# Kernel tuning notes

Hardware: AMD Instinct MI355X
Metric: run time of the kernel (lower is better)

Reference implementation:

```python
import jax, jax.numpy as jnp
import numpy as np

N = 100000      # n_nodes
E = 1600000     # n_edges (avg degree 16)
F_IN = 128      # nfeat
H = 128         # nhid
C = 64          # nclass


def setup_inputs() -> dict:
    key = jax.random.key(0)
    ks = jax.random.split(key, 6)
    x = jax.random.normal(ks[0], (N, F_IN), dtype=jnp.float32)
    edge_index = jax.random.randint(ks[1], (2, E), 0, N, dtype=jnp.int32)
    # Glorot-ish init for GCNConv weights, zeros for bias (PyG default)
    W1 = jax.random.normal(ks[2], (F_IN, H), dtype=jnp.float32) * (1.0 / np.sqrt(F_IN))
    b1 = jnp.zeros((H,), dtype=jnp.float32)
    W2 = jax.random.normal(ks[3], (H, C), dtype=jnp.float32) * (1.0 / np.sqrt(H))
    b2 = jnp.zeros((C,), dtype=jnp.float32)
    return {"x": x, "edge_index": edge_index, "W1": W1, "b1": b1, "W2": W2, "b2": b2}


def _gcn_conv(x, W, b, src, dst, n):
    """PyG GCNConv: h = W^T x, out_i = sum_j norm_ij * h_j + b, with
    symmetric normalization over the self-loop-augmented graph."""
    h = x @ W                                                   # [n, out]
    deg = jax.ops.segment_sum(jnp.ones(src.shape[0], h.dtype), dst, num_segments=n)
    dinv = jnp.where(deg > 0, jax.lax.rsqrt(deg), 0.0)          # D^-1/2
    norm = dinv[src] * dinv[dst]                                # [E+n]
    msg = h[src] * norm[:, None]                                # gather + scale
    out = jax.ops.segment_sum(msg, dst, num_segments=n)         # scatter-add
    return out + b


def reference(x, edge_index, W1, b1, W2, b2):
    loop = jnp.arange(N, dtype=edge_index.dtype)
    src = jnp.concatenate([edge_index[0], loop])  # sources j (with self loops)
    dst = jnp.concatenate([edge_index[1], loop])  # targets i
    h = jax.nn.relu(_gcn_conv(x, W1, b1, src, dst, N))  # dropout = identity (eval)
    out = _gcn_conv(h, W2, b2, src, dst, N)
    return jax.nn.log_softmax(out, axis=1)
```

## Files before the change

### kernel.cpp

```cpp
#include <hip/hip_runtime.h>
#include <hip/hip_fp16.h>
#include <cstdint>
#include <cstddef>
#include <cstring>


__device__ inline unsigned pack_bf16x2(float a, float b) {
    unsigned ua = __float_as_uint(a);
    unsigned ub = __float_as_uint(b);
    ua += 0x7fffu + ((ua >> 16) & 1u);
    ub += 0x7fffu + ((ub >> 16) & 1u);
    return (ua >> 16) | (ub & 0xffff0000u);
}
__device__ inline unsigned short bf16_rne(float v) {
    unsigned u = __float_as_uint(v);
    u += 0x7fffu + ((u >> 16) & 1u);
    return (unsigned short)(u >> 16);
}
__device__ inline float bf16lo(unsigned u) { return __uint_as_float(u << 16); }
__device__ inline float bf16hi(unsigned u) { return __uint_as_float(u & 0xffff0000u); }


typedef float fv2 __attribute__((ext_vector_type(2)));

template <bool HI>
__device__ inline fv2 fp8_fv2(unsigned u) {
#if __has_builtin(__builtin_amdgcn_cvt_pk_f32_fp8)
    return __builtin_amdgcn_cvt_pk_f32_fp8((int)u, HI);
#else
    unsigned u2 = HI ? (u >> 16) : (u & 0xffffu);
    unsigned w = (u2 & 0xFFu) | ((u2 & 0xFF00u) << 8);
    unsigned hb = ((w & 0x00800080u) << 8) | ((w & 0x007f007fu) << 7);
    __half2 h2;
    memcpy(&h2, &hb, 4);
    float2 f = __half22float2(h2);
    fv2 r;
    r.x = f.x * 256.0f;
    r.y = f.y * 256.0f;
    return r;
#endif
}

__device__ inline fv2 bfpair(unsigned u) {
    union { unsigned q[2]; fv2 f; } t;
    t.q[0] = u << 16;
    t.q[1] = u & 0xffff0000u;
    return t.f;
}

__device__ inline unsigned f32_to_fp8_byte(float v) {
    unsigned short hb = __half_as_ushort(__float2half(v * 0.00390625f));
    unsigned t = hb & 0x7fffu;
    t += 0x3fu + ((t >> 7) & 1u);
    return ((hb >> 8) & 0x80u) | (t >> 7);
}

__device__ inline unsigned char f32_to_fp8_b(float v) {
#if __has_builtin(__builtin_amdgcn_cvt_pk_fp8_f32)
    return (unsigned char)(__builtin_amdgcn_cvt_pk_fp8_f32(v, v, 0, false) & 0xff);
#else
    return (unsigned char)f32_to_fp8_byte(v);
#endif
}

typedef int iv4 __attribute__((ext_vector_type(4)));

#define NPART 8
#define KB    32
#define NPP_MAX 12500


__global__ void k_zero16(int* __restrict__ p) {
    if (threadIdx.x < 16) p[threadIdx.x] = 0;
}

__global__ __launch_bounds__(256) void k_bcount(const int* __restrict__ dst,
                                                int* __restrict__ bucketCount,
                                                int E, int npp) {
    __shared__ int c8[NPART];
    if (threadIdx.x < NPART) c8[threadIdx.x] = 0;
    __syncthreads();
    int t = blockIdx.x * blockDim.x + threadIdx.x;
    int stride = gridDim.x * blockDim.x;
    int E4 = E >> 2;
    const iv4* d4 = (const iv4*)dst;
    for (int i = t; i < E4; i += stride) {
        iv4 d = d4[i];
        atomicAdd(&c8[(unsigned)d.x / (unsigned)npp], 1);
        atomicAdd(&c8[(unsigned)d.y / (unsigned)npp], 1);
        atomicAdd(&c8[(unsigned)d.z / (unsigned)npp], 1);
        atomicAdd(&c8[(unsigned)d.w / (unsigned)npp], 1);
    }
    for (int e = E4 * 4 + t; e < E; e += stride)
        atomicAdd(&c8[(unsigned)dst[e] / (unsigned)npp], 1);
    __syncthreads();
    if (threadIdx.x < NPART) atomicAdd(&bucketCount[threadIdx.x], c8[threadIdx.x]);
}

__global__ void k_bscan(const int* __restrict__ bucketCount,
                        int* __restrict__ bucketBase,
                        int* __restrict__ bucketCursor) {
    if (threadIdx.x == 0) {
        int run = 0;
        for (int p = 0; p < NPART; ++p) {
            bucketBase[p] = run;
            bucketCursor[p] = run;
            run += bucketCount[p];
        }
    }
}

__global__ __launch_bounds__(256) void k_bucket(const int* __restrict__ src,
                                                const int* __restrict__ dst,
                                                int* __restrict__ bucketCursor,
                                                int2* __restrict__ pairs,
                                                int E, int npp) {
    __shared__ int cnt8[NPART], run8[NPART], gbase8[NPART];
    int tid = threadIdx.x;
    int base_e = blockIdx.x * 4096 + tid * 16;
    int nv = min(16, E - base_e);
    if (nv < 0) nv = 0;
    int dv[16], sv[16];
    if (nv == 16) {
        for (int q = 0; q < 4; ++q) {
            iv4 d = *(const iv4*)(dst + base_e + q * 4);
            iv4 s = *(const iv4*)(src + base_e + q * 4);
            dv[q * 4 + 0] = d.x; dv[q * 4 + 1] = d.y; dv[q * 4 + 2] = d.z; dv[q * 4 + 3] = d.w;
            sv[q * 4 + 0] = s.x; sv[q * 4 + 1] = s.y; sv[q * 4 + 2] = s.z; sv[q * 4 + 3] = s.w;
        }
    } else {
        for (int k = 0; k < nv; ++k) { dv[k] = dst[base_e + k]; sv[k] = src[base_e + k]; }
    }
    if (tid < NPART) { cnt8[tid] = 0; run8[tid] = 0; }
    __syncthreads();
    for (int k = 0; k < nv; ++k)
        atomicAdd(&cnt8[(unsigned)dv[k] / (unsigned)npp], 1);
    __syncthreads();
    if (tid < NPART) gbase8[tid] = atomicAdd(&bucketCursor[tid], cnt8[tid]);
    __syncthreads();
    for (int k = 0; k < nv; ++k) {
        int p = (unsigned)dv[k] / (unsigned)npp;
        int r = atomicAdd(&run8[p], 1);
        int2 pr; pr.x = dv[k]; pr.y = sv[k];
        pairs[gbase8[p] + r] = pr;
    }
}

__global__ __launch_bounds__(256) void k_count_part(const int2* __restrict__ pairs,
                                                    const int* __restrict__ bucketBase,
                                                    const int* __restrict__ bucketCount,
                                                    int* __restrict__ cntarr, int npp) {
    __shared__ int h[NPP_MAX];
    int p = blockIdx.x & (NPART - 1);
    int b = blockIdx.x >> 3;
    int lo = p * npp;
    for (int i = threadIdx.x; i < npp; i += 256) h[i] = 0;
    __syncthreads();
    int segBase = bucketBase[p], sz = bucketCount[p];
    int chunk = (sz + KB - 1) / KB;
    int s0 = segBase + b * chunk;
    int s1 = min(segBase + sz, s0 + chunk);
    for (int i = s0 + threadIdx.x; i < s1; i += 256)
        atomicAdd(&h[pairs[i].x - lo], 1);
    __syncthreads();
    size_t out = (size_t)(p * KB + b) * npp;
    for (int i = threadIdx.x; i < npp; i += 256) cntarr[out + i] = h[i];
}

__global__ void k_indeg_scan(const int* __restrict__ cntarr,
                             float* __restrict__ dinv,
                             int* __restrict__ row_ptr,
                             int* __restrict__ partials, int n, int npp) {
    __shared__ int s[256];
    int t = threadIdx.x;
    int node0 = blockIdx.x * 1024 + t * 4;
    int v0 = 0, v1 = 0, v2 = 0, v3 = 0;
    if (((npp & 3) == 0) && (node0 + 3 < n) && (node0 / npp == (node0 + 3) / npp)) {
        int p = node0 / npp;
        int dl = node0 - p * npp;
        size_t base = (size_t)p * KB * npp + dl;
        for (int b = 0; b < KB; ++b) {
            iv4 c = *(const iv4*)(cntarr + base + (size_t)b * npp);
            v0 += c.x; v1 += c.y; v2 += c.z; v3 += c.w;
        }
    } else {
        for (int r = 0; r < 4; ++r) {
            int node = node0 + r;
            if (node < n) {
                int p = node / npp;
                int dl = node - p * npp;
                size_t base = (size_t)p * KB * npp + dl;
                int sum = 0;
                for (int b = 0; b < KB; ++b) sum += cntarr[base + (size_t)b * npp];
                if (r == 0) v0 = sum; else if (r == 1) v1 = sum;
                else if (r == 2) v2 = sum; else v3 = sum;
            }
        }
    }
    if (node0 + 0 < n) dinv[node0 + 0] = rsqrtf((float)v0 + 1.0f);
    if (node0 + 1 < n) dinv[node0 + 1] = rsqrtf((float)v1 + 1.0f);
    if (node0 + 2 < n) dinv[node0 + 2] = rsqrtf((float)v2 + 1.0f);
    if (node0 + 3 < n) dinv[node0 + 3] = rsqrtf((float)v3 + 1.0f);
    int sum = v0 + v1 + v2 + v3;
    s[t] = sum;
    __syncthreads();
    for (int off = 1; off < 256; off <<= 1) {
        int x = (t >= off) ? s[t - off] : 0;
        __syncthreads();
        s[t] += x;
        __syncthreads();
    }
    int excl = s[t] - sum;
    if ((node0 + 0) < n) row_ptr[node0 + 0] = excl;
    if ((node0 + 1) < n) row_ptr[node0 + 1] = excl + v0;
    if ((node0 + 2) < n) row_ptr[node0 + 2] = excl + v0 + v1;
    if ((node0 + 3) < n) row_ptr[node0 + 3] = excl + v0 + v1 + v2;
    if (t == 255) partials[blockIdx.x] = s[255];
}

__global__ void k_scan_partials(int* __restrict__ partials, int np) {
    __shared__ int s[256];
    int t = threadIdx.x;
    int v = (t < np) ? partials[t] : 0;
    s[t] = v;
    __syncthreads();
    for (int off = 1; off < 256; off <<= 1) {
        int x = (t >= off) ? s[t - off] : 0;
        __syncthreads();
        s[t] += x;
        __syncthreads();
    }
    if (t < np) partials[t] = s[t] - v;
}

__global__ void k_finalize_bases(int* __restrict__ row_ptr,
                                 const int* __restrict__ partials,
                                 int* __restrict__ cntarr, int n, int E, int npp) {
    int i = blockIdx.x * blockDim.x + threadIdx.x;
    if (i >= n) return;
    int rp = row_ptr[i] + partials[i >> 10];
    row_ptr[i] = rp;
    if (i == 0) row_ptr[n] = E;
    int p = (unsigned)i / (unsigned)npp;
    int dl = i - p * npp;
    size_t base = (size_t)p * KB * npp + dl;
    int run = rp;
    for (int b = 0; b < KB; ++b) {
        size_t idx = base + (size_t)b * npp;
        int c = cntarr[idx];
        cntarr[idx] = run;
        run += c;
    }
}

__global__ __launch_bounds__(256) void k_fill2(const int2* __restrict__ pairs,
                                               const int* __restrict__ bucketBase,
                                               const int* __restrict__ bucketCount,
                                               const int* __restrict__ cntarr,
                                               int* __restrict__ col, int npp) {
    __shared__ int cur[NPP_MAX];
    int p = blockIdx.x & (NPART - 1);
    int b = blockIdx.x >> 3;
    int lo = p * npp;
    size_t slice = (size_t)(p * KB + b) * npp;
    for (int i = threadIdx.x; i < npp; i += 256) cur[i] = cntarr[slice + i];
    __syncthreads();
    int segBase = bucketBase[p], sz = bucketCount[p];
    int chunk = (sz + KB - 1) / KB;
    int s0 = segBase + b * chunk;
    int s1 = min(segBase + sz, s0 + chunk);
    for (int i = s0 + threadIdx.x; i < s1; i += 256) {
        int2 e = pairs[i];
        int pos = atomicAdd(&cur[e.x - lo], 1);
        col[pos] = e.y;
    }
}

typedef __attribute__((ext_vector_type(8))) short short8;
typedef __attribute__((ext_vector_type(4))) float f32x4;

union FragU {
    short8 s;
    uint4 u4;
    unsigned u[4];
};

template <int NOUT>
__global__ void k_packW(const float* __restrict__ W, unsigned* __restrict__ Bp) {
    const int NT = NOUT / 16;
    int nf = 4 * NT * 64;
    for (int fid = threadIdx.x; fid < nf; fid += 256) {
        int q = fid / (NT * 64);
        int rem = fid - q * NT * 64;
        int nt = rem >> 6;
        int lane = rem & 63;
        int k0 = q * 32 + (lane >> 4) * 8;
        int ncol = nt * 16 + (lane & 15);
        unsigned u[4];
        for (int h = 0; h < 4; ++h) {
            float a = W[(k0 + 2 * h) * NOUT + ncol];
            float b = W[(k0 + 2 * h + 1) * NOUT + ncol];
            u[h] = pack_bf16x2(a, b);
        }
        uint4 o = {u[0], u[1], u[2], u[3]};
        *(uint4*)(Bp + (size_t)fid * 4) = o;
    }
}

__global__ __launch_bounds__(256) void k_gemm128_mfma(const float* __restrict__ X,
                                                      const unsigned* __restrict__ Bp,
                                                      const float* __restrict__ dinv,
                                                      unsigned char* __restrict__ H8,
                                                      int n) {
    int w = threadIdx.x >> 6;
    int lane = threadIdx.x & 63;
    int quad = lane >> 4;
    int lrow = lane & 15;
    int row0 = blockIdx.x * 64 + w * 16;
    int rowA = min(row0 + lrow, n - 1);

    f32x4 acc[8];
    for (int nt = 0; nt < 8; ++nt) acc[nt] = (f32x4){0.f, 0.f, 0.f, 0.f};

    for (int q = 0; q < 4; ++q) {
        const float* xp = X + (size_t)rowA * 128 + q * 32 + quad * 8;
        float4 x0 = *(const float4*)xp;
        float4 x1 = *(const float4*)(xp + 4);
        FragU a;
        a.u[0] = pack_bf16x2(x0.x, x0.y);
        a.u[1] = pack_bf16x2(x0.z, x0.w);
        a.u[2] = pack_bf16x2(x1.x, x1.y);
        a.u[3] = pack_bf16x2(x1.z, x1.w);
        for (int nt = 0; nt < 8; ++nt) {
            FragU b;
            b.u4 = *(const uint4*)(Bp + ((size_t)(q * 8 + nt) * 64 + lane) * 4);
            acc[nt] = __builtin_amdgcn_mfma_f32_16x16x32_bf16(a.s, b.s, acc[nt], 0, 0, 0);
        }
    }

    int rbase = row0 + quad * 4;
    float dv[4];
    if (rbase + 3 < n) {
        float4 d4 = *(const float4*)(dinv + rbase);
        dv[0] = d4.x; dv[1] = d4.y; dv[2] = d4.z; dv[3] = d4.w;
    } else {
        for (int r = 0; r < 4; ++r) dv[r] = dinv[min(rbase + r, n - 1)];
    }
    for (int nt = 0; nt < 8; ++nt) {
        for (int r = 0; r < 4; ++r) {
            int row = rbase + r;
            if (row < n)
                H8[(size_t)row * 128 + nt * 16 + lrow] = f32_to_fp8_b(dv[r] * acc[nt][r]);
        }
    }
}

__global__ __launch_bounds__(256) void k_gemm64_mfma(const unsigned* __restrict__ Xb,
                                                     const unsigned* __restrict__ Bp,
                                                     const float* __restrict__ dinv,
                                                     unsigned short* __restrict__ H16,
                                                     int n) {
    int w = threadIdx.x >> 6;
    int lane = threadIdx.x & 63;
    int quad = lane >> 4;
    int lrow = lane & 15;
    int row0 = blockIdx.x * 64 + w * 16;
    int rowA = min(row0 + lrow, n - 1);

    f32x4 acc[4];
    for (int nt = 0; nt < 4; ++nt) acc[nt] = (f32x4){0.f, 0.f, 0.f, 0.f};

    for (int q = 0; q < 4; ++q) {
        FragU a;
        a.u4 = *(const uint4*)(Xb + (size_t)rowA * 64 + q * 16 + quad * 4);
        for (int nt = 0; nt < 4; ++nt) {
            FragU b;
            b.u4 = *(const uint4*)(Bp + ((size_t)(q * 4 + nt) * 64 + lane) * 4);
            acc[nt] = __builtin_amdgcn_mfma_f32_16x16x32_bf16(a.s, b.s, acc[nt], 0, 0, 0);
        }
    }

    int rbase = row0 + quad * 4;
    float dv[4];
    if (rbase + 3 < n) {
        float4 d4 = *(const float4*)(dinv + rbase);
        dv[0] = d4.x; dv[1] = d4.y; dv[2] = d4.z; dv[3] = d4.w;
    } else {
        for (int r = 0; r < 4; ++r) dv[r] = dinv[min(rbase + r, n - 1)];
    }
    for (int nt = 0; nt < 4; ++nt) {
        for (int r = 0; r < 4; ++r) {
            int row = rbase + r;
            if (row < n)
                H16[(size_t)row * 64 + nt * 16 + lrow] = bf16_rne(dv[r] * acc[nt][r]);
        }
    }
}


__global__ __launch_bounds__(256) void k_agg_relu(const unsigned* __restrict__ hs,
                                                  const float* __restrict__ dinv,
                                                  const int* __restrict__ row_ptr,
                                                  const int* __restrict__ col,
                                                  const float* __restrict__ bias,
                                                  unsigned* __restrict__ out, int n) {
    int node = blockIdx.x * 16 + (threadIdx.x >> 4);
    if (node >= n) return;
    int l = threadIdx.x & 15;
    const uint2* hrow = (const uint2*)hs;
    fv2 a0 = {0.f, 0.f}, a1 = {0.f, 0.f}, a2 = {0.f, 0.f}, a3 = {0.f, 0.f};
    {
        uint2 u = hrow[(size_t)node * 16 + l];
        a0 += fp8_fv2<false>(u.x); a1 += fp8_fv2<true>(u.x);
        a2 += fp8_fv2<false>(u.y); a3 += fp8_fv2<true>(u.y);
    }
    int k = row_ptr[node], p1 = row_ptr[node + 1];
    for (; k + 8 <= p1; k += 8) {
        int cA = col[k + 0], cB = col[k + 1], cC = col[k + 2], cD = col[k + 3];
        int cE = col[k + 4], cF = col[k + 5], cG = col[k + 6], cH = col[k + 7];
        uint2 uA = hrow[(size_t)cA * 16 + l];
        uint2 uB = hrow[(size_t)cB * 16 + l];
        uint2 uC = hrow[(size_t)cC * 16 + l];
        uint2 uD = hrow[(size_t)cD * 16 + l];
        uint2 uE = hrow[(size_t)cE * 16 + l];
        uint2 uF = hrow[(size_t)cF * 16 + l];
        uint2 uG = hrow[(size_t)cG * 16 + l];
        uint2 uH = hrow[(size_t)cH * 16 + l];
        a0 += fp8_fv2<false>(uA.x); a1 += fp8_fv2<true>(uA.x);
        a2 += fp8_fv2<false>(uA.y); a3 += fp8_fv2<true>(uA.y);
        a0 += fp8_fv2<false>(uB.x); a1 += fp8_fv2<true>(uB.x);
        a2 += fp8_fv2<false>(uB.y); a3 += fp8_fv2<true>(uB.y);
        a0 += fp8_fv2<false>(uC.x); a1 += fp8_fv2<true>(uC.x);
        a2 += fp8_fv2<false>(uC.y); a3 += fp8_fv2<true>(uC.y);
        a0 += fp8_fv2<false>(uD.x); a1 += fp8_fv2<true>(uD.x);
        a2 += fp8_fv2<false>(uD.y); a3 += fp8_fv2<true>(uD.y);
        a0 += fp8_fv2<false>(uE.x); a1 += fp8_fv2<true>(uE.x);
        a2 += fp8_fv2<false>(uE.y); a3 += fp8_fv2<true>(uE.y);
        a0 += fp8_fv2<false>(uF.x); a1 += fp8_fv2<true>(uF.x);
        a2 += fp8_fv2<false>(uF.y); a3 += fp8_fv2<true>(uF.y);
        a0 += fp8_fv2<false>(uG.x); a1 += fp8_fv2<true>(uG.x);
        a2 += fp8_fv2<false>(uG.y); a3 += fp8_fv2<true>(uG.y);
        a0 += fp8_fv2<false>(uH.x); a1 += fp8_fv2<true>(uH.x);
        a2 += fp8_fv2<false>(uH.y); a3 += fp8_fv2<true>(uH.y);
    }
    for (; k + 4 <= p1; k += 4) {
        int cA = col[k + 0], cB = col[k + 1], cC = col[k + 2], cD = col[k + 3];
        uint2 uA = hrow[(size_t)cA * 16 + l];
        uint2 uB = hrow[(size_t)cB * 16 + l];
        uint2 uC = hrow[(size_t)cC * 16 + l];
        uint2 uD = hrow[(size_t)cD * 16 + l];
        a0 += fp8_fv2<false>(uA.x); a1 += fp8_fv2<true>(uA.x);
        a2 += fp8_fv2<false>(uA.y); a3 += fp8_fv2<true>(uA.y);
        a0 += fp8_fv2<false>(uB.x); a1 += fp8_fv2<true>(uB.x);
        a2 += fp8_fv2<false>(uB.y); a3 += fp8_fv2<true>(uB.y);
        a0 += fp8_fv2<false>(uC.x); a1 += fp8_fv2<true>(uC.x);
        a2 += fp8_fv2<false>(uC.y); a3 += fp8_fv2<true>(uC.y);
        a0 += fp8_fv2<false>(uD.x); a1 += fp8_fv2<true>(uD.x);
        a2 += fp8_fv2<false>(uD.y); a3 += fp8_fv2<true>(uD.y);
    }
    for (; k < p1; ++k) {
        int j = col[k];
        uint2 u = hrow[(size_t)j * 16 + l];
        a0 += fp8_fv2<false>(u.x); a1 += fp8_fv2<true>(u.x);
        a2 += fp8_fv2<false>(u.y); a3 += fp8_fv2<true>(u.y);
    }
    float di = dinv[node];
    float4 b4a = *(const float4*)(bias + 8 * l);
    float4 b4b = *(const float4*)(bias + 8 * l + 4);
    float v0 = fmaf(di, a0.x, b4a.x);
    float v1 = fmaf(di, a0.y, b4a.y);
    float v2 = fmaf(di, a1.x, b4a.z);
    float v3 = fmaf(di, a1.y, b4a.w);
    float v4 = fmaf(di, a2.x, b4b.x);
    float v5 = fmaf(di, a2.y, b4b.y);
    float v6 = fmaf(di, a3.x, b4b.z);
    float v7 = fmaf(di, a3.y, b4b.w);
    v0 = v0 > 0.f ? v0 : 0.f;
    v1 = v1 > 0.f ? v1 : 0.f;
    v2 = v2 > 0.f ? v2 : 0.f;
    v3 = v3 > 0.f ? v3 : 0.f;
    v4 = v4 > 0.f ? v4 : 0.f;
    v5 = v5 > 0.f ? v5 : 0.f;
    v6 = v6 > 0.f ? v6 : 0.f;
    v7 = v7 > 0.f ? v7 : 0.f;
    uint4 o = {pack_bf16x2(v0, v1), pack_bf16x2(v2, v3),
               pack_bf16x2(v4, v5), pack_bf16x2(v6, v7)};
    *(uint4*)(out + (size_t)node * 64 + 4 * l) = o;
}

__global__ __launch_bounds__(256) void k_agg_lsm(const unsigned* __restrict__ hs,
                                                 const float* __restrict__ dinv,
                                                 const int* __restrict__ row_ptr,
                                                 const int* __restrict__ col,
                                                 const float* __restrict__ bias,
                                                 float* __restrict__ out, int n) {
    int node = blockIdx.x * 16 + (threadIdx.x >> 4);
    if (node >= n) return;
    int l = threadIdx.x & 15;
    const uint2* hrow = (const uint2*)hs;
    fv2 aX = {0.f, 0.f}, aY = {0.f, 0.f};
    {
        uint2 u = hrow[(size_t)node * 16 + l];
        aX += bfpair(u.x);
        aY += bfpair(u.y);
    }
    int k = row_ptr[node], p1 = row_ptr[node + 1];
    for (; k + 8 <= p1; k += 8) {
        int cA = col[k + 0], cB = col[k + 1], cC = col[k + 2], cD = col[k + 3];
        int cE = col[k + 4], cF = col[k + 5], cG = col[k + 6], cH = col[k + 7];
        uint2 uA = hrow[(size_t)cA * 16 + l];
        uint2 uB = hrow[(size_t)cB * 16 + l];
        uint2 uC = hrow[(size_t)cC * 16 + l];
        uint2 uD = hrow[(size_t)cD * 16 + l];
        uint2 uE = hrow[(size_t)cE * 16 + l];
        uint2 uF = hrow[(size_t)cF * 16 + l];
        uint2 uG = hrow[(size_t)cG * 16 + l];
        uint2 uH = hrow[(size_t)cH * 16 + l];
        aX += bfpair(uA.x); aY += bfpair(uA.y);
        aX += bfpair(uB.x); aY += bfpair(uB.y);
        aX += bfpair(uC.x); aY += bfpair(uC.y);
        aX += bfpair(uD.x); aY += bfpair(uD.y);
        aX += bfpair(uE.x); aY += bfpair(uE.y);
        aX += bfpair(uF.x); aY += bfpair(uF.y);
        aX += bfpair(uG.x); aY += bfpair(uG.y);
        aX += bfpair(uH.x); aY += bfpair(uH.y);
    }
    for (; k + 4 <= p1; k += 4) {
        int cA = col[k + 0], cB = col[k + 1], cC = col[k + 2], cD = col[k + 3];
        uint2 uA = hrow[(size_t)cA * 16 + l];
        uint2 uB = hrow[(size_t)cB * 16 + l];
        uint2 uC = hrow[(size_t)cC * 16 + l];
        uint2 uD = hrow[(size_t)cD * 16 + l];
        aX += bfpair(uA.x); aY += bfpair(uA.y);
        aX += bfpair(uB.x); aY += bfpair(uB.y);
        aX += bfpair(uC.x); aY += bfpair(uC.y);
        aX += bfpair(uD.x); aY += bfpair(uD.y);
    }
    for (; k < p1; ++k) {
        int j = col[k];
        uint2 u = hrow[(size_t)j * 16 + l];
        aX += bfpair(u.x); aY += bfpair(u.y);
    }
    float di = dinv[node];
    float4 b4 = *(const float4*)(bias + 4 * l);
    float v0 = fmaf(di, aX.x, b4.x);
    float v1 = fmaf(di, aX.y, b4.y);
    float v2 = fmaf(di, aY.x, b4.z);
    float v3 = fmaf(di, aY.y, b4.w);
    float m = fmaxf(fmaxf(v0, v1), fmaxf(v2, v3));
    for (int off = 8; off; off >>= 1) m = fmaxf(m, __shfl_xor(m, off));
    float s = __expf(v0 - m) + __expf(v1 - m) + __expf(v2 - m) + __expf(v3 - m);
    for (int off = 8; off; off >>= 1) s += __shfl_xor(s, off);
    float ls = __logf(s);
    float4 o = {v0 - m - ls, v1 - m - ls, v2 - m - ls, v3 - m - ls};
    *(float4*)(out + (size_t)node * 64 + 4 * l) = o;
}


extern "C" void kernel_launch(void* const* d_in, const int* in_sizes, int n_in,
                              void* d_out, int out_size, void* d_ws, size_t ws_size,
                              hipStream_t stream) {
    const float* x  = (const float*)d_in[0];
    const int*   ei = (const int*)d_in[1];
    const float* W1 = (const float*)d_in[2];
    const float* b1 = (const float*)d_in[3];
    const float* W2 = (const float*)d_in[4];
    const float* b2 = (const float*)d_in[5];
    float* out = (float*)d_out;

    const int N = in_sizes[0] / 128;
    const int E = in_sizes[1] / 2;
    const int* src = ei;
    const int* dst = ei + E;
    const int npp = (N + NPART - 1) / NPART;

    char* w = (char*)d_ws;
    size_t off = 0;
    auto alloc = [&](size_t bytes) -> void* {
        void* p = w + off;
        off += (bytes + 255) & ~(size_t)255;
        return p;
    };
    int*      row_ptr  = (int*)alloc((size_t)(N + 1) * 4);
    int*      colarr   = (int*)alloc((size_t)E * 4);
    int*      partials = (int*)alloc(256 * 4);
    int*      bmeta    = (int*)alloc(16 * 4);
    int*      bbase    = (int*)alloc(NPART * 4);
    float*    dinv     = (float*)alloc((size_t)N * 4);
    unsigned* h1f8     = (unsigned*)alloc((size_t)N * 32 * 4);
    unsigned* a1b      = (unsigned*)alloc((size_t)N * 64 * 4);
    unsigned* h2b      = (unsigned*)alloc((size_t)N * 32 * 4);
    unsigned* Bp1      = (unsigned*)alloc(4 * 8 * 64 * 16);
    unsigned* Bp2      = (unsigned*)alloc(4 * 4 * 64 * 16);
    int2* pairs  = (int2*)a1b;
    int*  cntarr = (int*)((char*)a1b + (size_t)E * 8);
    (void)ws_size; (void)n_in; (void)out_size;

    int* bucketCount  = bmeta;
    int* bucketCursor = bmeta + 8;
    int nscan = (N + 1023) / 1024;
    int nA3 = (E + 4095) / 4096;
    int ngemm = (N + 63) / 64;

    k_zero16<<<1, 64, 0, stream>>>(bmeta);
    k_packW<128><<<1, 256, 0, stream>>>(W1, Bp1);
    k_packW<64><<<1, 256, 0, stream>>>(W2, Bp2);
    k_bcount<<<256, 256, 0, stream>>>(dst, bucketCount, E, npp);
    k_bscan<<<1, 64, 0, stream>>>(bucketCount, bbase, bucketCursor);
    k_bucket<<<nA3, 256, 0, stream>>>(src, dst, bucketCursor, pairs, E, npp);
    k_count_part<<<NPART * KB, 256, 0, stream>>>(pairs, bbase, bucketCount, cntarr, npp);
    k_indeg_scan<<<nscan, 256, 0, stream>>>(cntarr, dinv, row_ptr, partials, N, npp);
    k_scan_partials<<<1, 256, 0, stream>>>(partials, nscan);
    k_finalize_bases<<<(N + 255) / 256, 256, 0, stream>>>(row_ptr, partials, cntarr,
                                                          N, E, npp);
    k_fill2<<<NPART * KB, 256, 0, stream>>>(pairs, bbase, bucketCount, cntarr,
                                            colarr, npp);

    k_gemm128_mfma<<<ngemm, 256, 0, stream>>>(x, Bp1, dinv, (unsigned char*)h1f8, N);
    k_agg_relu<<<(N + 15) / 16, 256, 0, stream>>>(h1f8, dinv, row_ptr, colarr, b1, a1b, N);
    k_gemm64_mfma<<<ngemm, 256, 0, stream>>>(a1b, Bp2, dinv, (unsigned short*)h2b, N);
    k_agg_lsm<<<(N + 15) / 16, 256, 0, stream>>>(h2b, dinv, row_ptr, colarr, b2, out, N);
}
```

Baseline: 274.2 us.

## Replace count-scan-bucket pipeline with single-pass ballot bucketing into fixed-capacity packed partitions

Result: no change. 269.3 us (-1.8%).

```diff
diff --git a/kernel.cpp b/kernel.cpp
--- a/kernel.cpp
+++ b/kernel.cpp
@@ -17,8 +17,6 @@
     u += 0x7fffu + ((u >> 16) & 1u);
     return (unsigned short)(u >> 16);
 }
-__device__ inline float bf16lo(unsigned u) { return __uint_as_float(u << 16); }
-__device__ inline float bf16hi(unsigned u) { return __uint_as_float(u & 0xffff0000u); }
 
 
 typedef float fv2 __attribute__((ext_vector_type(2)));
@@ -68,100 +66,99 @@
 #define NPART 8
 #define KB    32
 #define NPP_MAX 12500
-
-
-__global__ void k_zero16(int* __restrict__ p) {
-    if (threadIdx.x < 16) p[threadIdx.x] = 0;
-}
-
-__global__ __launch_bounds__(256) void k_bcount(const int* __restrict__ dst,
-                                                int* __restrict__ bucketCount,
-                                                int E, int npp) {
-    __shared__ int c8[NPART];
-    if (threadIdx.x < NPART) c8[threadIdx.x] = 0;
+#define EB    2048
+
+
+__global__ __launch_bounds__(256) void k_bucket_ballot(const int* __restrict__ src,
+                                                       const int* __restrict__ dst,
+                                                       int* __restrict__ cursor8,
+                                                       unsigned* __restrict__ pairs,
+                                                       int E, int npp, int capE,
+                                                       int srcb) {
+    __shared__ int sWcnt[4][NPART];
+    __shared__ int sWoff[4][NPART];
+    int tid = threadIdx.x;
+    int wv = tid >> 6;
+    int lane = tid & 63;
+    int base_e = blockIdx.x * EB + tid * 8;
+    int nv = min(8, E - base_e);
+    if (nv < 0) nv = 0;
+    int dv[8], sv[8];
+    if (nv == 8) {
+        *(iv4*)(dv + 0) = *(const iv4*)(dst + base_e + 0);
+        *(iv4*)(dv + 4) = *(const iv4*)(dst + base_e + 4);
+        *(iv4*)(sv + 0) = *(const iv4*)(src + base_e + 0);
+        *(iv4*)(sv + 4) = *(const iv4*)(src + base_e + 4);
+    } else {
+        for (int k = 0; k < 8; ++k) {
+            dv[k] = (k < nv) ? dst[base_e + k] : -1;
+            sv[k] = (k < nv) ? src[base_e + k] : 0;
+        }
+    }
+    unsigned long long below = (1ull << lane) - 1ull;
+    int wb[NPART];
+#pragma unroll
+    for (int pp = 0; pp < NPART; ++pp) wb[pp] = 0;
+    int pv[8], pos[8];
+#pragma unroll
+    for (int s = 0; s < 8; ++s) {
+        int d = dv[s];
+        int p = (d >= 0) ? (int)((unsigned)d / (unsigned)npp) : NPART;
+        pv[s] = p;
+        unsigned long long msel = 0;
+        int base = 0;
+#pragma unroll
+        for (int pp = 0; pp < NPART; ++pp) {
+            unsigned long long m = __ballot(p == pp);
+            if (p == pp) { msel = m; base = wb[pp]; }
+            wb[pp] += (int)__popcll(m);
+        }
+        pos[s] = base + (int)__popcll(msel & below);
+    }
+    if (lane < NPART) {
+        int v = 0;
+#pragma unroll
+        for (int pp = 0; pp < NPART; ++pp)
+            if (lane == pp) v = wb[pp];
+        sWcnt[wv][lane] = v;
+    }
     __syncthreads();
-    int t = blockIdx.x * blockDim.x + threadIdx.x;
-    int stride = gridDim.x * blockDim.x;
-    int E4 = E >> 2;
-    const iv4* d4 = (const iv4*)dst;
-    for (int i = t; i < E4; i += stride) {
-        iv4 d = d4[i];
-        atomicAdd(&c8[(unsigned)d.x / (unsigned)npp], 1);
-        atomicAdd(&c8[(unsigned)d.y / (unsigned)npp], 1);
-        atomicAdd(&c8[(unsigned)d.z / (unsigned)npp], 1);
-        atomicAdd(&c8[(unsigned)d.w / (unsigned)npp], 1);
-    }
-    for (int e = E4 * 4 + t; e < E; e += stride)
-        atomicAdd(&c8[(unsigned)dst[e] / (unsigned)npp], 1);
+    if (tid < NPART) {
+        int c0 = sWcnt[0][tid], c1 = sWcnt[1][tid], c2 = sWcnt[2][tid], c3 = sWcnt[3][tid];
+        int gb = atomicAdd(&cursor8[tid], c0 + c1 + c2 + c3);
+        sWoff[0][tid] = gb;
+        sWoff[1][tid] = gb + c0;
+        sWoff[2][tid] = gb + c0 + c1;
+        sWoff[3][tid] = gb + c0 + c1 + c2;
+    }
     __syncthreads();
-    if (threadIdx.x < NPART) atomicAdd(&bucketCount[threadIdx.x], c8[threadIdx.x]);
-}
-
-__global__ void k_bscan(const int* __restrict__ bucketCount,
-                        int* __restrict__ bucketBase,
-                        int* __restrict__ bucketCursor) {
-    if (threadIdx.x == 0) {
-        int run = 0;
-        for (int p = 0; p < NPART; ++p) {
-            bucketBase[p] = run;
-            bucketCursor[p] = run;
-            run += bucketCount[p];
-        }
-    }
-}
-
-__global__ __launch_bounds__(256) void k_bucket(const int* __restrict__ src,
-                                                const int* __restrict__ dst,
-                                                int* __restrict__ bucketCursor,
-                                                int2* __restrict__ pairs,
-                                                int E, int npp) {
-    __shared__ int cnt8[NPART], run8[NPART], gbase8[NPART];
-    int tid = threadIdx.x;
-    int base_e = blockIdx.x * 4096 + tid * 16;
-    int nv = min(16, E - base_e);
-    if (nv < 0) nv = 0;
-    int dv[16], sv[16];
-    if (nv == 16) {
-        for (int q = 0; q < 4; ++q) {
-            iv4 d = *(const iv4*)(dst + base_e + q * 4);
-            iv4 s = *(const iv4*)(src + base_e + q * 4);
-            dv[q * 4 + 0] = d.x; dv[q * 4 + 1] = d.y; dv[q * 4 + 2] = d.z; dv[q * 4 + 3] = d.w;
-            sv[q * 4 + 0] = s.x; sv[q * 4 + 1] = s.y; sv[q * 4 + 2] = s.z; sv[q * 4 + 3] = s.w;
-        }
-    } else {
-        for (int k = 0; k < nv; ++k) { dv[k] = dst[base_e + k]; sv[k] = src[base_e + k]; }
-    }
-    if (tid < NPART) { cnt8[tid] = 0; run8[tid] = 0; }
-    __syncthreads();
-    for (int k = 0; k < nv; ++k)
-        atomicAdd(&cnt8[(unsigned)dv[k] / (unsigned)npp], 1);
-    __syncthreads();
-    if (tid < NPART) gbase8[tid] = atomicAdd(&bucketCursor[tid], cnt8[tid]);
-    __syncthreads();
-    for (int k = 0; k < nv; ++k) {
-        int p = (unsigned)dv[k] / (unsigned)npp;
-        int r = atomicAdd(&run8[p], 1);
-        int2 pr; pr.x = dv[k]; pr.y = sv[k];
-        pairs[gbase8[p] + r] = pr;
-    }
-}
-
-__global__ __launch_bounds__(256) void k_count_part(const int2* __restrict__ pairs,
-                                                    const int* __restrict__ bucketBase,
-                                                    const int* __restrict__ bucketCount,
-                                                    int* __restrict__ cntarr, int npp) {
+#pragma unroll
+    for (int s = 0; s < 8; ++s) {
+        int p = pv[s];
+        if (p < NPART) {
+            int off = sWoff[wv][p];
+            pairs[(size_t)p * capE + off + pos[s]] =
+                ((unsigned)(dv[s] - p * npp) << srcb) | (unsigned)sv[s];
+        }
+    }
+}
+
+__global__ __launch_bounds__(256) void k_count_part(const unsigned* __restrict__ pairs,
+                                                    const int* __restrict__ cursor8,
+                                                    int* __restrict__ cntarr,
+                                                    int npp, int capE, int srcb) {
     __shared__ int h[NPP_MAX];
     int p = blockIdx.x & (NPART - 1);
     int b = blockIdx.x >> 3;
-    int lo = p * npp;
     for (int i = threadIdx.x; i < npp; i += 256) h[i] = 0;
     __syncthreads();
-    int segBase = bucketBase[p], sz = bucketCount[p];
+    int sz = cursor8[p];
     int chunk = (sz + KB - 1) / KB;
-    int s0 = segBase + b * chunk;
-    int s1 = min(segBase + sz, s0 + chunk);
+    int s0 = b * chunk;
+    int s1 = min(sz, s0 + chunk);
+    const unsigned* seg = pairs + (size_t)p * capE;
     for (int i = s0 + threadIdx.x; i < s1; i += 256)
-        atomicAdd(&h[pairs[i].x - lo], 1);
+        atomicAdd(&h[seg[i] >> srcb], 1);
     __syncthreads();
     size_t out = (size_t)(p * KB + b) * npp;
     for (int i = threadIdx.x; i < npp; i += 256) cntarr[out + i] = h[i];
@@ -253,26 +250,27 @@
     }
 }
 
-__global__ __launch_bounds__(256) void k_fill2(const int2* __restrict__ pairs,
-                                               const int* __restrict__ bucketBase,
-                                               const int* __restrict__ bucketCount,
+__global__ __launch_bounds__(256) void k_fill2(const unsigned* __restrict__ pairs,
+                                               const int* __restrict__ cursor8,
                                                const int* __restrict__ cntarr,
-                                               int* __restrict__ col, int npp) {
+                                               int* __restrict__ col,
+                                               int npp, int capE, int srcb) {
     __shared__ int cur[NPP_MAX];
     int p = blockIdx.x & (NPART - 1);
     int b = blockIdx.x >> 3;
-    int lo = p * npp;
     size_t slice = (size_t)(p * KB + b) * npp;
     for (int i = threadIdx.x; i < npp; i += 256) cur[i] = cntarr[slice + i];
     __syncthreads();
-    int segBase = bucketBase[p], sz = bucketCount[p];
+    int sz = cursor8[p];
     int chunk = (sz + KB - 1) / KB;
-    int s0 = segBase + b * chunk;
-    int s1 = min(segBase + sz, s0 + chunk);
+    int s0 = b * chunk;
+    int s1 = min(sz, s0 + chunk);
+    const unsigned* seg = pairs + (size_t)p * capE;
+    unsigned smask = (1u << srcb) - 1u;
     for (int i = s0 + threadIdx.x; i < s1; i += 256) {
-        int2 e = pairs[i];
-        int pos = atomicAdd(&cur[e.x - lo], 1);
-        col[pos] = e.y;
+        unsigned u = seg[i];
+        int pos = atomicAdd(&cur[u >> srcb], 1);
+        col[pos] = (int)(u & smask);
     }
 }
 
@@ -285,9 +283,8 @@
     unsigned u[4];
 };
 
-template <int NOUT>
-__global__ void k_packW(const float* __restrict__ W, unsigned* __restrict__ Bp) {
-    const int NT = NOUT / 16;
+__device__ inline void packW_body(const float* __restrict__ W, unsigned* __restrict__ Bp,
+                                  int NOUT, int NT) {
     int nf = 4 * NT * 64;
     for (int fid = threadIdx.x; fid < nf; fid += 256) {
         int q = fid / (NT * 64);
@@ -305,6 +302,12 @@
         uint4 o = {u[0], u[1], u[2], u[3]};
         *(uint4*)(Bp + (size_t)fid * 4) = o;
     }
+}
+
+__global__ void k_packW2(const float* __restrict__ W1, unsigned* __restrict__ Bp1,
+                         const float* __restrict__ W2, unsigned* __restrict__ Bp2) {
+    if (blockIdx.x == 0) packW_body(W1, Bp1, 128, 8);
+    else                 packW_body(W2, Bp2, 64, 4);
 }
 
 __global__ __launch_bounds__(256) void k_gemm128_mfma(const float* __restrict__ X,
@@ -573,6 +576,9 @@
     const int* src = ei;
     const int* dst = ei + E;
     const int npp = (N + NPART - 1) / NPART;
+    const int capE = (E + NPART - 1) / NPART + 32768;
+    int srcb = 1;
+    while ((1 << srcb) < N) ++srcb;
 
     char* w = (char*)d_ws;
     size_t off = 0;
@@ -584,37 +590,33 @@
     int*      row_ptr  = (int*)alloc((size_t)(N + 1) * 4);
     int*      colarr   = (int*)alloc((size_t)E * 4);
     int*      partials = (int*)alloc(256 * 4);
-    int*      bmeta    = (int*)alloc(16 * 4);
-    int*      bbase    = (int*)alloc(NPART * 4);
+    int*      cursor8  = (int*)alloc(8 * 4);
     float*    dinv     = (float*)alloc((size_t)N * 4);
     unsigned* h1f8     = (unsigned*)alloc((size_t)N * 32 * 4);
     unsigned* a1b      = (unsigned*)alloc((size_t)N * 64 * 4);
     unsigned* h2b      = (unsigned*)alloc((size_t)N * 32 * 4);
     unsigned* Bp1      = (unsigned*)alloc(4 * 8 * 64 * 16);
     unsigned* Bp2      = (unsigned*)alloc(4 * 4 * 64 * 16);
-    int2* pairs  = (int2*)a1b;
-    int*  cntarr = (int*)((char*)a1b + (size_t)E * 8);
+    unsigned* pairsU   = (unsigned*)a1b;
+    int*      cntarr   = (int*)((char*)a1b + (size_t)NPART * capE * 4);
     (void)ws_size; (void)n_in; (void)out_size;
 
-    int* bucketCount  = bmeta;
-    int* bucketCursor = bmeta + 8;
     int nscan = (N + 1023) / 1024;
-    int nA3 = (E + 4095) / 4096;
+    int nbb = (E + EB - 1) / EB;
     int ngemm = (N + 63) / 64;
 
-    k_zero16<<<1, 64, 0, stream>>>(bmeta);
-    k_packW<128><<<1, 256, 0, stream>>>(W1, Bp1);
-    k_packW<64><<<1, 256, 0, stream>>>(W2, Bp2);
-    k_bcount<<<256, 256, 0, stream>>>(dst, bucketCount, E, npp);
-    k_bscan<<<1, 64, 0, stream>>>(bucketCount, bbase, bucketCursor);
-    k_bucket<<<nA3, 256, 0, stream>>>(src, dst, bucketCursor, pairs, E, npp);
-    k_count_part<<<NPART * KB, 256, 0, stream>>>(pairs, bbase, bucketCount, cntarr, npp);
+    hipMemsetAsync(cursor8, 0, 8 * 4, stream);
+    k_packW2<<<2, 256, 0, stream>>>(W1, Bp1, W2, Bp2);
+    k_bucket_ballot<<<nbb, 256, 0, stream>>>(src, dst, cursor8, pairsU,
+                                             E, npp, capE, srcb);
+    k_count_part<<<NPART * KB, 256, 0, stream>>>(pairsU, cursor8, cntarr,
+                                                 npp, capE, srcb);
     k_indeg_scan<<<nscan, 256, 0, stream>>>(cntarr, dinv, row_ptr, partials, N, npp);
     k_scan_partials<<<1, 256, 0, stream>>>(partials, nscan);
     k_finalize_bases<<<(N + 255) / 256, 256, 0, stream>>>(row_ptr, partials, cntarr,
                                                           N, E, npp);
-    k_fill2<<<NPART * KB, 256, 0, stream>>>(pairs, bbase, bucketCount, cntarr,
-                                            colarr, npp);
+    k_fill2<<<NPART * KB, 256, 0, stream>>>(pairsU, cursor8, cntarr, colarr,
+                                            npp, capE, srcb);
 
     k_gemm128_mfma<<<ngemm, 256, 0, stream>>>(x, Bp1, dinv, (unsigned char*)h1f8, N);
     k_agg_relu<<<(N + 15) / 16, 256, 0, stream>>>(h1f8, dinv, row_ptr, colarr, b1, a1b, N);
```
